# Kernel optimization log

Hardware: AMD Instinct MI355X
Metric: run time of the kernel (lower is better)

Reference implementation:

```python
import jax, jax.numpy as jnp
import numpy as np

N = 50000
E = 800000
IN_C = 128
HID = 64
HEADS = 4
EPS = 1e-5
NEG_SLOPE = 0.2


def _glorot(key, shape, fan_in):
    return jax.random.normal(key, shape, dtype=jnp.float32) / np.sqrt(fan_in)


def setup_inputs() -> dict:
    key = jax.random.key(0)
    ks = jax.random.split(key, 32)
    d = {}
    d["x"] = jax.random.normal(ks[0], (N, IN_C), dtype=jnp.float32)
    d["edge_index"] = jax.random.randint(ks[1], (2, E), 0, N, dtype=jnp.int32)
    ph = HID // HEADS  # per-head channels for concat layers (16)
    # Layer 1: in -> [heads, ph], concat
    d["W1"] = _glorot(ks[2], (IN_C, HEADS * ph), IN_C)
    d["a1s"] = _glorot(ks[3], (HEADS, ph), ph)
    d["a1d"] = _glorot(ks[4], (HEADS, ph), ph)
    d["b1"] = jnp.zeros((HID,), jnp.float32)
    # Layer 2: hid -> [heads, ph], concat
    d["W2"] = _glorot(ks[5], (HID, HEADS * ph), HID)
    d["a2s"] = _glorot(ks[6], (HEADS, ph), ph)
    d["a2d"] = _glorot(ks[7], (HEADS, ph), ph)
    d["b2"] = jnp.zeros((HID,), jnp.float32)
    # Layer 3: hid -> [heads, HID], mean over heads (concat=False)
    d["W3"] = _glorot(ks[8], (HID, HEADS * HID), HID)
    d["a3s"] = _glorot(ks[9], (HEADS, HID), HID)
    d["a3d"] = _glorot(ks[10], (HEADS, HID), HID)
    d["b3"] = jnp.zeros((HID,), jnp.float32)
    # BatchNorms (eval mode: running stats)
    for i, k0 in zip((1, 2, 3), (11, 14, 17)):
        d[f"bn{i}_g"] = jnp.ones((HID,), jnp.float32)
        d[f"bn{i}_b"] = jnp.zeros((HID,), jnp.float32)
        d[f"bn{i}_m"] = 0.1 * jax.random.normal(ks[k0], (HID,), dtype=jnp.float32)
        d[f"bn{i}_v"] = jax.random.uniform(ks[k0 + 1], (HID,), minval=0.5, maxval=1.5, dtype=jnp.float32)
    # Classifier MLP: HID -> HID//2 -> 1
    d["cW1"] = _glorot(ks[20], (HID, HID // 2), HID)
    d["cb1"] = jnp.zeros((HID // 2,), jnp.float32)
    d["cW2"] = _glorot(ks[21], (HID // 2, 1), HID // 2)
    d["cb2"] = jnp.zeros((1,), jnp.float32)
    return d


def _gat_layer(x, src, dst, W, a_s, a_d, b, concat):
    n = x.shape[0]
    heads, outc = a_s.shape
    h = (x @ W).reshape(n, heads, outc)           # [N,H,C]
    al_s = jnp.einsum("nhc,hc->nh", h, a_s)       # [N,H]
    al_d = jnp.einsum("nhc,hc->nh", h, a_d)
    e = jax.nn.leaky_relu(al_s[src] + al_d[dst], NEG_SLOPE)  # [E,H]
    m = jax.ops.segment_max(e, dst, num_segments=n)
    ex = jnp.exp(e - m[dst])
    den = jax.ops.segment_sum(ex, dst, num_segments=n)
    alpha = ex / den[dst]                          # segment softmax over dst
    out = jax.ops.segment_sum(h[src] * alpha[..., None], dst, num_segments=n)  # [N,H,C]
    if concat:
        out = out.reshape(n, heads * outc)
    else:
        out = out.mean(axis=1)
    return out + b


def _bn(x, g, b, m, v):
    return g * (x - m) * jax.lax.rsqrt(v + EPS) + b


def reference(x, edge_index, W1, a1s, a1d, b1, W2, a2s, a2d, b2, W3, a3s, a3d, b3,
              bn1_g, bn1_b, bn1_m, bn1_v, bn2_g, bn2_b, bn2_m, bn2_v,
              bn3_g, bn3_b, bn3_m, bn3_v, cW1, cb1, cW2, cb2):
    n = x.shape[0]
    # PyG GATConv adds self-loops by default
    loop = jnp.arange(n, dtype=edge_index.dtype)
    src = jnp.concatenate([edge_index[0], loop])
    dst = jnp.concatenate([edge_index[1], loop])

    h = _gat_layer(x, src, dst, W1, a1s, a1d, b1, concat=True)
    h = jax.nn.elu(_bn(h, bn1_g, bn1_b, bn1_m, bn1_v))
    h = _gat_layer(h, src, dst, W2, a2s, a2d, b2, concat=True)
    h = jax.nn.elu(_bn(h, bn2_g, bn2_b, bn2_m, bn2_v))
    h = _gat_layer(h, src, dst, W3, a3s, a3d, b3, concat=False)
    h = _bn(h, bn3_g, bn3_b, bn3_m, bn3_v)

    h = jax.nn.elu(h @ cW1 + cb1)
    out = (h @ cW2 + cb2).squeeze(-1)  # [N]
    return out
```

## Files before the change

### kernel.cpp

```cpp
#include <hip/hip_runtime.h>

#define HH 4

__device__ __forceinline__ float lrelu(float v){ return v > 0.f ? v : 0.2f*v; }

template<int C>
__global__ void gemm_gat(const float* __restrict__ X, const float* __restrict__ W,
                         const float* __restrict__ a_s, const float* __restrict__ a_d,
                         float* __restrict__ h, float* __restrict__ als, float* __restrict__ ald,
                         int IC) {
    const int OC = 4*C;
    int n = blockIdx.x;
    int t = threadIdx.x;
    __shared__ float xs[128];
    for (int k = t; k < IC; k += OC) xs[k] = X[(size_t)n*IC + k];
    __syncthreads();
    float acc = 0.f;
    for (int k = 0; k < IC; ++k) acc += xs[k] * W[k*OC + t];
    h[(size_t)n*OC + t] = acc;
    int hh = t / C, c = t % C;
    float ps = acc * a_s[hh*C + c];
    float pd = acc * a_d[hh*C + c];
    #pragma unroll
    for (int m = 1; m < C; m <<= 1) { ps += __shfl_xor(ps, m); pd += __shfl_xor(pd, m); }
    if (c == 0) { als[n*HH + hh] = ps; ald[n*HH + hh] = pd; }
}


__global__ void zero_i32(int* __restrict__ p, int n){
    int i = blockIdx.x*256 + threadIdx.x;
    if (i < n) p[i] = 0;
}

__global__ void count_deg(const int* __restrict__ ei, int* __restrict__ deg, int E){
    int e = blockIdx.x*256 + threadIdx.x;
    if (e < E) atomicAdd(&deg[ei[E + e]], 1);
}

__global__ void deg_bsum(const int* __restrict__ deg, int* __restrict__ bsum, int N){
    int t = threadIdx.x;
    int base = blockIdx.x*1024 + t*4;
    int s = 0;
    if (base + 3 < N){
        int4 v = *(const int4*)(deg + base);
        s = v.x + v.y + v.z + v.w;
    } else {
        for (int q = 0; q < 4; ++q) if (base + q < N) s += deg[base + q];
    }
    #pragma unroll
    for (int m = 1; m < 64; m <<= 1) s += __shfl_xor(s, m);
    __shared__ int ws[4];
    if ((t & 63) == 0) ws[t >> 6] = s;
    __syncthreads();
    if (t == 0) bsum[blockIdx.x] = ws[0] + ws[1] + ws[2] + ws[3];
}

__global__ void scan_write(const int* __restrict__ deg, const int* __restrict__ bsum,
                           int* __restrict__ row_off, int* __restrict__ cursor, int N, int E){
    int t = threadIdx.x, bid = blockIdx.x, lane = t & 63, w = t >> 6;
    int base = bid*1024 + t*4;
    int v0 = 0, v1 = 0, v2 = 0, v3 = 0;
    if (base + 3 < N){
        int4 v = *(const int4*)(deg + base);
        v0 = v.x; v1 = v.y; v2 = v.z; v3 = v.w;
    } else {
        if (base     < N) v0 = deg[base];
        if (base + 1 < N) v1 = deg[base + 1];
        if (base + 2 < N) v2 = deg[base + 2];
        if (base + 3 < N) v3 = deg[base + 3];
    }
    int s = v0 + v1 + v2 + v3;
    int x = s;
    #pragma unroll
    for (int d = 1; d < 64; d <<= 1){
        int y = __shfl_up(x, d);
        if (lane >= d) x += y;
    }
    __shared__ int wsum[4];
    __shared__ int boff_s;
    if (lane == 63) wsum[w] = x;
    if (t < 64){
        int o = 0;
        for (int i = t; i < bid; i += 64) o += bsum[i];
        #pragma unroll
        for (int m = 1; m < 64; m <<= 1) o += __shfl_xor(o, m);
        if (t == 0) boff_s = o;
    }
    __syncthreads();
    int woff = 0;
    for (int i = 0; i < w; ++i) woff += wsum[i];
    int o = boff_s + woff + (x - s);
    if (base     < N){ row_off[base]     = o; cursor[base]     = o; o += v0; }
    if (base + 1 < N){ row_off[base + 1] = o; cursor[base + 1] = o; o += v1; }
    if (base + 2 < N){ row_off[base + 2] = o; cursor[base + 2] = o; o += v2; }
    if (base + 3 < N){ row_off[base + 3] = o; cursor[base + 3] = o; o += v3; }
    if (t == 0 && bid == 0) row_off[N] = E;
}

__global__ void fill_csr(const int* __restrict__ ei, int* __restrict__ cursor,
                         int* __restrict__ ssrc, int E){
    int e = blockIdx.x*256 + threadIdx.x;
    if (e < E){
        int d = ei[E + e];
        int p = atomicAdd(&cursor[d], 1);
        ssrc[p] = ei[e];
    }
}

__global__ void prep_l3(const float* __restrict__ W3, const float* __restrict__ a3s,
                        const float* __restrict__ a3d, float* __restrict__ ws3,
                        float* __restrict__ wd3, float* __restrict__ W3p){
    int t = threadIdx.x;
    int hh = t >> 6, k = t & 63;
    float ss = 0.f, sd = 0.f;
    for (int c = 0; c < 64; ++c){
        float w = W3[k*256 + hh*64 + c];
        ss += w * a3s[hh*64 + c];
        sd += w * a3d[hh*64 + c];
        W3p[t*64 + c] = 0.25f * w;
    }
    ws3[t] = ss; wd3[t] = sd;
}

template<bool L3PREP>
__global__ void gat_agg16(const int* __restrict__ row_off, const int* __restrict__ ssrc,
                          const float* __restrict__ als, const float* __restrict__ ald,
                          const float* __restrict__ h, const float* __restrict__ b,
                          const float* __restrict__ g, const float* __restrict__ bb,
                          const float* __restrict__ bm, const float* __restrict__ bv,
                          float* __restrict__ out,
                          const float* __restrict__ ws3, const float* __restrict__ wd3,
                          float* __restrict__ als3, float* __restrict__ ald3, int N){
    int lane = threadIdx.x & 63;
    int n = blockIdx.x*4 + (threadIdx.x >> 6);
    if (n >= N) return;
    int hh = lane >> 4, j = lane & 15;
    float ad = ald[n*HH + hh];
    float vself = __expf(lrelu(als[n*HH + hh] + ad));
    int beg = row_off[n], end = row_off[n+1];
    float denp = 0.f;
    float acc = vself * h[(size_t)n*64 + lane];
    for (int cb = beg; cb < end; cb += 16){
        int e = cb + j;
        int s = n; float ev = 0.f;
        if (e < end){ s = ssrc[e]; ev = __expf(lrelu(als[s*HH + hh] + ad)); }
        denp += ev;
        int cn = min(16, end - cb);
        int grp = lane & 48;
        for (int q = 0; q < cn; ++q){
            float w = __shfl(ev, grp | q);
            int  sq = __shfl(s,  grp | q);
            acc += w * h[(size_t)sq*64 + lane];
        }
    }
    #pragma unroll
    for (int m = 1; m < 16; m <<= 1) denp += __shfl_xor(denp, m);
    float den = vself + denp;
    float val = acc/den + b[lane];
    val = g[lane]*(val - bm[lane])*rsqrtf(bv[lane] + 1e-5f) + bb[lane];
    val = val > 0.f ? val : expm1f(val);
    out[(size_t)n*64 + lane] = val;
    if (L3PREP){
        #pragma unroll
        for (int jj = 0; jj < 4; ++jj){
            float ps = val * ws3[jj*64 + lane];
            float pd = val * wd3[jj*64 + lane];
            #pragma unroll
            for (int mm = 1; mm < 64; mm <<= 1){
                ps += __shfl_xor(ps, mm);
                pd += __shfl_xor(pd, mm);
            }
            if (lane == 0){ als3[n*HH + jj] = ps; ald3[n*HH + jj] = pd; }
        }
    }
}

__global__ void gat_agg3(const int* __restrict__ row_off, const int* __restrict__ ssrc,
                         const float* __restrict__ als, const float* __restrict__ ald,
                         const float* __restrict__ hin, float* __restrict__ y, int N){
    int lane = threadIdx.x & 63;
    int n = blockIdx.x*4 + (threadIdx.x >> 6);
    if (n >= N) return;
    float4 ad = *(const float4*)(ald + n*4);
    float4 av = *(const float4*)(als + n*4);
    float v0 = __expf(lrelu(av.x + ad.x)), v1 = __expf(lrelu(av.y + ad.y));
    float v2 = __expf(lrelu(av.z + ad.z)), v3 = __expf(lrelu(av.w + ad.w));
    int beg = row_off[n], end = row_off[n+1];
    float hv = hin[(size_t)n*64 + lane];
    float acc0 = v0*hv, acc1 = v1*hv, acc2 = v2*hv, acc3 = v3*hv;
    float dp0 = 0.f, dp1 = 0.f, dp2 = 0.f, dp3 = 0.f;
    for (int cb = beg; cb < end; cb += 64){
        int e = cb + lane;
        int s = n; float e0 = 0.f, e1 = 0.f, e2 = 0.f, e3 = 0.f;
        if (e < end){
            s = ssrc[e];
            float4 a = *(const float4*)(als + s*4);
            e0 = __expf(lrelu(a.x + ad.x));
            e1 = __expf(lrelu(a.y + ad.y));
            e2 = __expf(lrelu(a.z + ad.z));
            e3 = __expf(lrelu(a.w + ad.w));
        }
        dp0 += e0; dp1 += e1; dp2 += e2; dp3 += e3;
        int cn = min(64, end - cb);
        for (int q = 0; q < cn; ++q){
            float w0 = __shfl(e0, q), w1 = __shfl(e1, q);
            float w2 = __shfl(e2, q), w3 = __shfl(e3, q);
            int  sq = __shfl(s, q);
            float hs = hin[(size_t)sq*64 + lane];
            acc0 += w0*hs; acc1 += w1*hs; acc2 += w2*hs; acc3 += w3*hs;
        }
    }
    #pragma unroll
    for (int m = 1; m < 64; m <<= 1){
        dp0 += __shfl_xor(dp0, m); dp1 += __shfl_xor(dp1, m);
        dp2 += __shfl_xor(dp2, m); dp3 += __shfl_xor(dp3, m);
    }
    float d0 = v0 + dp0, d1 = v1 + dp1, d2 = v2 + dp2, d3 = v3 + dp3;
    size_t base = (size_t)n*256 + lane;
    y[base]       = acc0/d0;
    y[base + 64]  = acc1/d1;
    y[base + 128] = acc2/d2;
    y[base + 192] = acc3/d3;
}

__global__ void post_l3(const float* __restrict__ y, const float* __restrict__ W3p,
                        const float* __restrict__ b, const float* __restrict__ g,
                        const float* __restrict__ bb, const float* __restrict__ bm,
                        const float* __restrict__ bv, float* __restrict__ out, int N){
    __shared__ float ys[16*256];
    int t = threadIdx.x;
    int n0 = blockIdx.x*16;
    for (int i = t; i < 16*256; i += 256){
        int nl = i >> 8, j = i & 255;
        int n = n0 + nl;
        ys[i] = (n < N) ? y[(size_t)n*256 + j] : 0.f;
    }
    __syncthreads();
    int c = t & 63, nb = t >> 6;
    float acc[4] = {0.f, 0.f, 0.f, 0.f};
    for (int j = 0; j < 256; ++j){
        float w = W3p[j*64 + c];
        #pragma unroll
        for (int q = 0; q < 4; ++q)
            acc[q] += ys[(nb + 4*q)*256 + j] * w;
    }
    float scale = g[c]*rsqrtf(bv[c] + 1e-5f);
    #pragma unroll
    for (int q = 0; q < 4; ++q){
        int n = n0 + nb + 4*q;
        if (n < N){
            float val = acc[q] + b[c];
            out[(size_t)n*64 + c] = scale*(val - bm[c]) + bb[c];
        }
    }
}

__global__ void classifier(const float* __restrict__ hin, const float* __restrict__ cW1,
                           const float* __restrict__ cb1, const float* __restrict__ cW2,
                           const float* __restrict__ cb2, float* __restrict__ out, int N){
    __shared__ float w1[64*32];
    __shared__ float b1s[32], w2[32];
    int t = threadIdx.x;
    for (int k = t; k < 64*32; k += 256) w1[k] = cW1[k];
    if (t < 32) { b1s[t] = cb1[t]; w2[t] = cW2[t]; }
    __syncthreads();
    int n = blockIdx.x*256 + t;
    if (n >= N) return;
    float hrow[64];
    #pragma unroll
    for (int k = 0; k < 64; ++k) hrow[k] = hin[(size_t)n*64 + k];
    float acc2 = cb2[0];
    #pragma unroll 4
    for (int j = 0; j < 32; ++j) {
        float a = b1s[j];
        #pragma unroll
        for (int k = 0; k < 64; ++k) a += hrow[k]*w1[k*32 + j];
        float e = a > 0.f ? a : expm1f(a);
        acc2 += e * w2[j];
    }
    out[n] = acc2;
}

extern "C" void kernel_launch(void* const* d_in, const int* in_sizes, int n_in,
                              void* d_out, int out_size, void* d_ws, size_t ws_size,
                              hipStream_t stream) {
    const float* x    = (const float*)d_in[0];
    const int*   ei   = (const int*)  d_in[1];
    const float* W1   = (const float*)d_in[2];
    const float* a1s  = (const float*)d_in[3];
    const float* a1d  = (const float*)d_in[4];
    const float* b1   = (const float*)d_in[5];
    const float* W2   = (const float*)d_in[6];
    const float* a2s  = (const float*)d_in[7];
    const float* a2d  = (const float*)d_in[8];
    const float* b2   = (const float*)d_in[9];
    const float* W3   = (const float*)d_in[10];
    const float* a3s  = (const float*)d_in[11];
    const float* a3d  = (const float*)d_in[12];
    const float* b3   = (const float*)d_in[13];
    const float* bn1g = (const float*)d_in[14];
    const float* bn1b = (const float*)d_in[15];
    const float* bn1m = (const float*)d_in[16];
    const float* bn1v = (const float*)d_in[17];
    const float* bn2g = (const float*)d_in[18];
    const float* bn2b = (const float*)d_in[19];
    const float* bn2m = (const float*)d_in[20];
    const float* bn2v = (const float*)d_in[21];
    const float* bn3g = (const float*)d_in[22];
    const float* bn3b = (const float*)d_in[23];
    const float* bn3m = (const float*)d_in[24];
    const float* bn3v = (const float*)d_in[25];
    const float* cW1  = (const float*)d_in[26];
    const float* cb1  = (const float*)d_in[27];
    const float* cW2  = (const float*)d_in[28];
    const float* cb2  = (const float*)d_in[29];

    const int N = in_sizes[0] / 128;
    const int E = in_sizes[1] / 2;

    float* h    = (float*)d_ws;
    float* hin  = h    + (size_t)N*64;
    float* y    = hin  + (size_t)N*64;
    float* als  = y    + (size_t)N*256;
    float* ald  = als  + (size_t)N*4;
    float* als3 = ald  + (size_t)N*4;
    float* ald3 = als3 + (size_t)N*4;
    float* ws3  = ald3 + (size_t)N*4;
    float* wd3  = ws3  + 256;
    float* W3p  = wd3  + 256;
    int* deg     = (int*)(W3p + 16384);
    int* row_off = deg + N;
    int* cursor  = row_off + (N + 1);
    int* ssrc    = cursor + N;
    int* bsum    = ssrc + E;

    const int B = 256;
    int gN  = (N + B-1)/B;
    int gE  = (E + B-1)/B;
    int NB  = (N + 1023)/1024;

    zero_i32<<<gN, B, 0, stream>>>(deg, N);
    count_deg<<<gE, B, 0, stream>>>(ei, deg, E);
    deg_bsum<<<NB, B, 0, stream>>>(deg, bsum, N);
    scan_write<<<NB, B, 0, stream>>>(deg, bsum, row_off, cursor, N, E);
    fill_csr<<<gE, B, 0, stream>>>(ei, cursor, ssrc, E);
    prep_l3<<<1, 256, 0, stream>>>(W3, a3s, a3d, ws3, wd3, W3p);

    gemm_gat<16><<<N, 64, 0, stream>>>(x, W1, a1s, a1d, h, als, ald, 128);
    gat_agg16<false><<<(N + 3)/4, B, 0, stream>>>(row_off, ssrc, als, ald, h, b1,
                                                  bn1g, bn1b, bn1m, bn1v, hin,
                                                  nullptr, nullptr, nullptr, nullptr, N);

    gemm_gat<16><<<N, 64, 0, stream>>>(hin, W2, a2s, a2d, h, als, ald, 64);
    gat_agg16<true><<<(N + 3)/4, B, 0, stream>>>(row_off, ssrc, als, ald, h, b2,
                                                 bn2g, bn2b, bn2m, bn2v, hin,
                                                 ws3, wd3, als3, ald3, N);

    gat_agg3<<<(N + 3)/4, B, 0, stream>>>(row_off, ssrc, als3, ald3, hin, y, N);
    post_l3<<<(N + 15)/16, B, 0, stream>>>(y, W3p, b3, bn3g, bn3b, bn3m, bn3v, h, N);

    classifier<<<gN, B, 0, stream>>>(h, cW1, cb1, cW2, cb2, (float*)d_out, N);
}
```

Baseline: 469.8 us.

## Fuse layer-3 aggregation with projection and batch gathers in aggregation loops

Layer-3 aggregation now does the per-head 256→64 projection, bias and batch norm itself, using a shared-memory tile per node. This removes the N×256 intermediate buffer and the separate post_l3 kernel. Both aggregation kernels now issue their neighbour row gathers in batches of eight, so several loads are in flight at once. gemm_gat now handles four nodes per 256-thread block with a per-wave shared-memory row instead of one 64-thread block per node. The trade-off is some wasted loads on padded edge slots, plus one full-block barrier in the fused kernel.

```diff
diff --git a/kernel.cpp b/kernel.cpp
--- a/kernel.cpp
+++ b/kernel.cpp
@@ -4,26 +4,28 @@
 
 __device__ __forceinline__ float lrelu(float v){ return v > 0.f ? v : 0.2f*v; }
 
-template<int C>
+template<int IC>
 __global__ void gemm_gat(const float* __restrict__ X, const float* __restrict__ W,
                          const float* __restrict__ a_s, const float* __restrict__ a_d,
                          float* __restrict__ h, float* __restrict__ als, float* __restrict__ ald,
-                         int IC) {
-    const int OC = 4*C;
-    int n = blockIdx.x;
-    int t = threadIdx.x;
-    __shared__ float xs[128];
-    for (int k = t; k < IC; k += OC) xs[k] = X[(size_t)n*IC + k];
-    __syncthreads();
+                         int N) {
+    int t = threadIdx.x, lane = t & 63, wid = t >> 6;
+    int n = blockIdx.x*4 + wid;
+    bool valid = n < N;
+    int nc = valid ? n : N-1;
+    __shared__ float xs[4][IC];
+    #pragma unroll
+    for (int k = lane; k < IC; k += 64) xs[wid][k] = X[(size_t)nc*IC + k];
     float acc = 0.f;
-    for (int k = 0; k < IC; ++k) acc += xs[k] * W[k*OC + t];
-    h[(size_t)n*OC + t] = acc;
-    int hh = t / C, c = t % C;
-    float ps = acc * a_s[hh*C + c];
-    float pd = acc * a_d[hh*C + c];
-    #pragma unroll
-    for (int m = 1; m < C; m <<= 1) { ps += __shfl_xor(ps, m); pd += __shfl_xor(pd, m); }
-    if (c == 0) { als[n*HH + hh] = ps; ald[n*HH + hh] = pd; }
+    #pragma unroll 8
+    for (int k = 0; k < IC; ++k) acc += xs[wid][k] * W[k*64 + lane];
+    if (valid) h[(size_t)nc*64 + lane] = acc;
+    int hh = lane >> 4, c = lane & 15;
+    float ps = acc * a_s[hh*16 + c];
+    float pd = acc * a_d[hh*16 + c];
+    #pragma unroll
+    for (int m = 1; m < 16; m <<= 1){ ps += __shfl_xor(ps, m); pd += __shfl_xor(pd, m); }
+    if (valid && c == 0){ als[nc*HH + hh] = ps; ald[nc*HH + hh] = pd; }
 }
 
 
@@ -134,7 +136,7 @@
     int lane = threadIdx.x & 63;
     int n = blockIdx.x*4 + (threadIdx.x >> 6);
     if (n >= N) return;
-    int hh = lane >> 4, j = lane & 15;
+    int hh = lane >> 4, j = lane & 15, grp = lane & 48;
     float ad = ald[n*HH + hh];
     float vself = __expf(lrelu(als[n*HH + hh] + ad));
     int beg = row_off[n], end = row_off[n+1];
@@ -145,12 +147,15 @@
         int s = n; float ev = 0.f;
         if (e < end){ s = ssrc[e]; ev = __expf(lrelu(als[s*HH + hh] + ad)); }
         denp += ev;
-        int cn = min(16, end - cb);
-        int grp = lane & 48;
-        for (int q = 0; q < cn; ++q){
-            float w = __shfl(ev, grp | q);
-            int  sq = __shfl(s,  grp | q);
-            acc += w * h[(size_t)sq*64 + lane];
+        #pragma unroll
+        for (int qb = 0; qb < 16; qb += 8){
+            int sq[8]; float hv[8];
+            #pragma unroll
+            for (int i = 0; i < 8; ++i) sq[i] = __shfl(s, grp | (qb + i));
+            #pragma unroll
+            for (int i = 0; i < 8; ++i) hv[i] = h[(size_t)sq[i]*64 + lane];
+            #pragma unroll
+            for (int i = 0; i < 8; ++i) acc += __shfl(ev, grp | (qb + i)) * hv[i];
         }
     }
     #pragma unroll
@@ -175,19 +180,22 @@
     }
 }
 
-__global__ void gat_agg3(const int* __restrict__ row_off, const int* __restrict__ ssrc,
-                         const float* __restrict__ als, const float* __restrict__ ald,
-                         const float* __restrict__ hin, float* __restrict__ y, int N){
-    int lane = threadIdx.x & 63;
-    int n = blockIdx.x*4 + (threadIdx.x >> 6);
-    if (n >= N) return;
-    float4 ad = *(const float4*)(ald + n*4);
-    float4 av = *(const float4*)(als + n*4);
-    float v0 = __expf(lrelu(av.x + ad.x)), v1 = __expf(lrelu(av.y + ad.y));
-    float v2 = __expf(lrelu(av.z + ad.z)), v3 = __expf(lrelu(av.w + ad.w));
+__global__ void gat_agg3_fused(const int* __restrict__ row_off, const int* __restrict__ ssrc,
+                               const float* __restrict__ als, const float* __restrict__ ald,
+                               const float* __restrict__ hin, const float* __restrict__ W3p,
+                               const float* __restrict__ b, const float* __restrict__ g,
+                               const float* __restrict__ bb, const float* __restrict__ bm,
+                               const float* __restrict__ bv, float* __restrict__ out, int N){
+    int t = threadIdx.x, lane = t & 63, wid = t >> 6;
+    int n0 = blockIdx.x*4;
+    int n = min(n0 + wid, N-1);
+    float4 adv = *(const float4*)(ald + n*4);
+    float4 av  = *(const float4*)(als + n*4);
+    float v0 = __expf(lrelu(av.x + adv.x)), v1 = __expf(lrelu(av.y + adv.y));
+    float v2 = __expf(lrelu(av.z + adv.z)), v3 = __expf(lrelu(av.w + adv.w));
     int beg = row_off[n], end = row_off[n+1];
-    float hv = hin[(size_t)n*64 + lane];
-    float acc0 = v0*hv, acc1 = v1*hv, acc2 = v2*hv, acc3 = v3*hv;
+    float hv0 = hin[(size_t)n*64 + lane];
+    float acc0 = v0*hv0, acc1 = v1*hv0, acc2 = v2*hv0, acc3 = v3*hv0;
     float dp0 = 0.f, dp1 = 0.f, dp2 = 0.f, dp3 = 0.f;
     for (int cb = beg; cb < end; cb += 64){
         int e = cb + lane;
@@ -195,19 +203,26 @@
         if (e < end){
             s = ssrc[e];
             float4 a = *(const float4*)(als + s*4);
-            e0 = __expf(lrelu(a.x + ad.x));
-            e1 = __expf(lrelu(a.y + ad.y));
-            e2 = __expf(lrelu(a.z + ad.z));
-            e3 = __expf(lrelu(a.w + ad.w));
+            e0 = __expf(lrelu(a.x + adv.x));
+            e1 = __expf(lrelu(a.y + adv.y));
+            e2 = __expf(lrelu(a.z + adv.z));
+            e3 = __expf(lrelu(a.w + adv.w));
         }
         dp0 += e0; dp1 += e1; dp2 += e2; dp3 += e3;
         int cn = min(64, end - cb);
-        for (int q = 0; q < cn; ++q){
-            float w0 = __shfl(e0, q), w1 = __shfl(e1, q);
-            float w2 = __shfl(e2, q), w3 = __shfl(e3, q);
-            int  sq = __shfl(s, q);
-            float hs = hin[(size_t)sq*64 + lane];
-            acc0 += w0*hs; acc1 += w1*hs; acc2 += w2*hs; acc3 += w3*hs;
+        for (int qb = 0; qb < cn; qb += 8){
+            int sq[8]; float hv[8];
+            #pragma unroll
+            for (int i = 0; i < 8; ++i) sq[i] = __shfl(s, qb + i);
+            #pragma unroll
+            for (int i = 0; i < 8; ++i) hv[i] = hin[(size_t)sq[i]*64 + lane];
+            #pragma unroll
+            for (int i = 0; i < 8; ++i){
+                acc0 += __shfl(e0, qb + i)*hv[i];
+                acc1 += __shfl(e1, qb + i)*hv[i];
+                acc2 += __shfl(e2, qb + i)*hv[i];
+                acc3 += __shfl(e3, qb + i)*hv[i];
+            }
         }
     }
     #pragma unroll
@@ -215,43 +230,25 @@
         dp0 += __shfl_xor(dp0, m); dp1 += __shfl_xor(dp1, m);
         dp2 += __shfl_xor(dp2, m); dp3 += __shfl_xor(dp3, m);
     }
-    float d0 = v0 + dp0, d1 = v1 + dp1, d2 = v2 + dp2, d3 = v3 + dp3;
-    size_t base = (size_t)n*256 + lane;
-    y[base]       = acc0/d0;
-    y[base + 64]  = acc1/d1;
-    y[base + 128] = acc2/d2;
-    y[base + 192] = acc3/d3;
-}
-
-__global__ void post_l3(const float* __restrict__ y, const float* __restrict__ W3p,
-                        const float* __restrict__ b, const float* __restrict__ g,
-                        const float* __restrict__ bb, const float* __restrict__ bm,
-                        const float* __restrict__ bv, float* __restrict__ out, int N){
-    __shared__ float ys[16*256];
-    int t = threadIdx.x;
-    int n0 = blockIdx.x*16;
-    for (int i = t; i < 16*256; i += 256){
-        int nl = i >> 8, j = i & 255;
-        int n = n0 + nl;
-        ys[i] = (n < N) ? y[(size_t)n*256 + j] : 0.f;
-    }
+    __shared__ __align__(16) float ysh[4*256];
+    ysh[wid*256 +   0 + lane] = acc0/(v0 + dp0);
+    ysh[wid*256 +  64 + lane] = acc1/(v1 + dp1);
+    ysh[wid*256 + 128 + lane] = acc2/(v2 + dp2);
+    ysh[wid*256 + 192 + lane] = acc3/(v3 + dp3);
     __syncthreads();
-    int c = t & 63, nb = t >> 6;
-    float acc[4] = {0.f, 0.f, 0.f, 0.f};
-    for (int j = 0; j < 256; ++j){
-        float w = W3p[j*64 + c];
-        #pragma unroll
-        for (int q = 0; q < 4; ++q)
-            acc[q] += ys[(nb + 4*q)*256 + j] * w;
-    }
-    float scale = g[c]*rsqrtf(bv[c] + 1e-5f);
-    #pragma unroll
-    for (int q = 0; q < 4; ++q){
-        int n = n0 + nb + 4*q;
-        if (n < N){
-            float val = acc[q] + b[c];
-            out[(size_t)n*64 + c] = scale*(val - bm[c]) + bb[c];
-        }
+    float accp = 0.f;
+    #pragma unroll 8
+    for (int jb = 0; jb < 256; jb += 4){
+        float4 yv = *(const float4*)&ysh[wid*256 + jb];
+        accp += yv.x * W3p[(jb    )*64 + lane];
+        accp += yv.y * W3p[(jb + 1)*64 + lane];
+        accp += yv.z * W3p[(jb + 2)*64 + lane];
+        accp += yv.w * W3p[(jb + 3)*64 + lane];
+    }
+    int nw = n0 + wid;
+    if (nw < N){
+        float val = accp + b[lane];
+        out[(size_t)nw*64 + lane] = g[lane]*(val - bm[lane])*rsqrtf(bv[lane] + 1e-5f) + bb[lane];
     }
 }
 
@@ -320,8 +317,7 @@
 
     float* h    = (float*)d_ws;
     float* hin  = h    + (size_t)N*64;
-    float* y    = hin  + (size_t)N*64;
-    float* als  = y    + (size_t)N*256;
+    float* als  = hin  + (size_t)N*64;
     float* ald  = als  + (size_t)N*4;
     float* als3 = ald  + (size_t)N*4;
     float* ald3 = als3 + (size_t)N*4;
@@ -338,6 +334,7 @@
     int gN  = (N + B-1)/B;
     int gE  = (E + B-1)/B;
     int NB  = (N + 1023)/1024;
+    int gN4 = (N + 3)/4;
 
     zero_i32<<<gN, B, 0, stream>>>(deg, N);
     count_deg<<<gE, B, 0, stream>>>(ei, deg, E);
@@ -346,18 +343,18 @@
     fill_csr<<<gE, B, 0, stream>>>(ei, cursor, ssrc, E);
     prep_l3<<<1, 256, 0, stream>>>(W3, a3s, a3d, ws3, wd3, W3p);
 
-    gemm_gat<16><<<N, 64, 0, stream>>>(x, W1, a1s, a1d, h, als, ald, 128);
-    gat_agg16<false><<<(N + 3)/4, B, 0, stream>>>(row_off, ssrc, als, ald, h, b1,
-                                                  bn1g, bn1b, bn1m, bn1v, hin,
-                                                  nullptr, nullptr, nullptr, nullptr, N);
-
-    gemm_gat<16><<<N, 64, 0, stream>>>(hin, W2, a2s, a2d, h, als, ald, 64);
-    gat_agg16<true><<<(N + 3)/4, B, 0, stream>>>(row_off, ssrc, als, ald, h, b2,
-                                                 bn2g, bn2b, bn2m, bn2v, hin,
-                                                 ws3, wd3, als3, ald3, N);
-
-    gat_agg3<<<(N + 3)/4, B, 0, stream>>>(row_off, ssrc, als3, ald3, hin, y, N);
-    post_l3<<<(N + 15)/16, B, 0, stream>>>(y, W3p, b3, bn3g, bn3b, bn3m, bn3v, h, N);
+    gemm_gat<128><<<gN4, B, 0, stream>>>(x, W1, a1s, a1d, h, als, ald, N);
+    gat_agg16<false><<<gN4, B, 0, stream>>>(row_off, ssrc, als, ald, h, b1,
+                                            bn1g, bn1b, bn1m, bn1v, hin,
+                                            nullptr, nullptr, nullptr, nullptr, N);
+
+    gemm_gat<64><<<gN4, B, 0, stream>>>(hin, W2, a2s, a2d, h, als, ald, N);
+    gat_agg16<true><<<gN4, B, 0, stream>>>(row_off, ssrc, als, ald, h, b2,
+                                           bn2g, bn2b, bn2m, bn2v, hin,
+                                           ws3, wd3, als3, ald3, N);
+
+    gat_agg3_fused<<<gN4, B, 0, stream>>>(row_off, ssrc, als3, ald3, hin, W3p,
+                                          b3, bn3g, bn3b, bn3m, bn3v, h, N);
 
     classifier<<<gN, B, 0, stream>>>(h, cW1, cb1, cW2, cb2, (float*)d_out, N);
 }
```

Measured after the change: 420.7 us. -10.4%, faster.
